# Kernel optimization log

Hardware: AMD Instinct MI355X
Metric: run time of the kernel (lower is better)

Reference implementation:

```python
import jax, jax.numpy as jnp
import numpy as np

N_NODES = 100000
N_EDGES = 3200000
N_FEAT = 128
EMB = 64
HID = 64
N_SUB = 500000
N_GRAPHS = 1024
BN_EPS = 1e-5


def setup_inputs() -> dict:
    key = jax.random.key(0)
    ks = jax.random.split(key, 12)
    full_x = jax.random.normal(ks[0], (N_NODES, N_FEAT), dtype=jnp.float32)
    full_edge_index = jax.random.randint(ks[1], (2, N_EDGES), 0, N_NODES, dtype=jnp.int64)
    subgraph_node_indices = jax.random.randint(ks[2], (N_SUB,), 0, N_NODES, dtype=jnp.int64)
    batch_vector = jax.random.randint(ks[3], (N_SUB,), 0, N_GRAPHS, dtype=jnp.int64)
    # GCNConv params (glorot-style scale)
    W_enc = jax.random.normal(ks[4], (N_FEAT, EMB), dtype=jnp.float32) * (1.0 / np.sqrt(N_FEAT))
    b_enc = jnp.zeros((EMB,), dtype=jnp.float32)
    # predictor MLP params
    W1 = jax.random.normal(ks[5], (EMB, HID), dtype=jnp.float32) * (1.0 / np.sqrt(EMB))
    b1 = jnp.zeros((HID,), dtype=jnp.float32)
    gamma = jnp.ones((HID,), dtype=jnp.float32)
    beta = jnp.zeros((HID,), dtype=jnp.float32)
    W2 = jax.random.normal(ks[6], (HID, 1), dtype=jnp.float32) * (1.0 / np.sqrt(HID))
    b2 = jnp.zeros((1,), dtype=jnp.float32)
    return {
        "full_x": full_x,
        "full_edge_index": full_edge_index,
        "subgraph_node_indices": subgraph_node_indices,
        "batch_vector": batch_vector,
        "W_enc": W_enc, "b_enc": b_enc,
        "W1": W1, "b1": b1, "gamma": gamma, "beta": beta,
        "W2": W2, "b2": b2,
    }


def gcn_conv(x, edge_index, W, b):
    # PyG GCNConv: add self-loops, symmetric degree normalization, linear transform
    n = x.shape[0]
    loops = jnp.arange(n, dtype=edge_index.dtype)
    row = jnp.concatenate([edge_index[0], loops])  # source
    col = jnp.concatenate([edge_index[1], loops])  # target
    deg = jax.ops.segment_sum(jnp.ones_like(col, dtype=x.dtype), col, num_segments=n)
    dinv = jnp.where(deg > 0, jax.lax.rsqrt(deg), 0.0)
    norm = dinv[row] * dinv[col]  # [E+N]
    xw = x @ W  # transform first: [N, EMB]
    msgs = xw[row] * norm[:, None]
    out = jax.ops.segment_sum(msgs, col, num_segments=n)
    return out + b


def reference(full_x, full_edge_index, subgraph_node_indices, batch_vector,
              W_enc, b_enc, W1, b1, gamma, beta, W2, b2):
    # encoder + relu over all nodes
    h = jax.nn.relu(gcn_conv(full_x, full_edge_index, W_enc, b_enc))  # [N, EMB]
    # gather subgraph members
    sub = h[subgraph_node_indices]  # [N_SUB, EMB]
    # segment-mean pool into per-subgraph embeddings
    sums = jax.ops.segment_sum(sub, batch_vector, num_segments=N_GRAPHS)
    cnts = jax.ops.segment_sum(jnp.ones((sub.shape[0],), sub.dtype), batch_vector, num_segments=N_GRAPHS)
    pooled = sums / jnp.maximum(cnts, 1.0)[:, None]  # [N_GRAPHS, EMB]
    # predictor: Linear -> ReLU -> BatchNorm1d (training-mode batch stats) -> Linear
    z = jax.nn.relu(pooled @ W1 + b1)  # [N_GRAPHS, HID]
    mu = jnp.mean(z, axis=0)
    var = jnp.mean((z - mu) ** 2, axis=0)  # biased, as torch BN normalization
    zn = (z - mu) * jax.lax.rsqrt(var + BN_EPS) * gamma + beta
    return zn @ W2 + b2  # [N_GRAPHS, 1]
```

## Files before the change

### kernel.cpp

```cpp
#include <hip/hip_runtime.h>

#define N_NODES 100000
#define N_EDGES 3200000
#define N_FEAT 128
#define EMB 64
#define HID 64
#define N_SUB 500000
#define N_GRAPHS 1024
#define BN_EPS 1e-5f

#define NBKT 782
#define TILE 4096
#define NTILES 782
#define NGTILES 123
#define BKT_MAX 4864
#define GCAP 640

typedef __attribute__((ext_vector_type(8))) short short8;
typedef __attribute__((ext_vector_type(8))) unsigned short ushort8v;
typedef __attribute__((ext_vector_type(4))) float floatx4;

#define OFF_BCUR   0u
#define OFF_BCURG  4096u
#define OFF_BNSUM  8192u
#define ZERO_BYTES 8704u
#define OFF_DINV   12288u
#define OFF_OFFS   412672u
#define OFF_PAIRS  812672u
#define OFF_XWS    OFF_PAIRS
#define OFF_CSR    16027264u
#define OFF_SORTED 31241856u
#define OFF_H      33863296u
#define OFF_Z      46663296u

__device__ __forceinline__ bool is_bf(const unsigned* gamma_raw) {
  return (gamma_raw[0] & 0xFFFFu) != 0u;
}
__device__ __forceinline__ bool idx_is64(const int* subp) {
  return (subp[1] | subp[3] | subp[5] | subp[7]) == 0;
}
__device__ __forceinline__ int ld_idx(const int* p, long long i, bool w64) {
  return w64 ? p[2 * i] : p[i];
}
__device__ __forceinline__ float bf2f(ushort u) {
  union { unsigned i; float f; } v; v.i = ((unsigned)u) << 16; return v.f;
}
__device__ __forceinline__ ushort f2bf(float f) {
  union { float f; unsigned i; } v; v.f = f;
  unsigned lsb = (v.i >> 16) & 1u;
  v.i += 0x7FFFu + lsb;
  return (ushort)(v.i >> 16);
}
__device__ __forceinline__ float ld_f(const void* p, int i, bool bf) {
  return bf ? bf2f(((const ushort*)p)[i]) : ((const float*)p)[i];
}

__global__ void k_scatsort(const int* e, const int* subp, const int* batch,
                           int* bcur, unsigned* pairs, int* bcurg, int* sorted) {
  __shared__ char smem[38912];
  int* cnt   = (int*)smem;
  int* lscan = cnt + 1024;
  int* gbase = lscan + 1024;
  int* psum  = gbase + 1024;
  unsigned* stage = (unsigned*)(psum + 512);
  unsigned short* stgb = (unsigned short*)(stage + 4096);
  bool w64 = idx_is64(subp);
  int tid = threadIdx.x;
  bool edges = blockIdx.x < NTILES;
  int nb   = edges ? NBKT : N_GRAPHS;
  int base = edges ? blockIdx.x * TILE : (blockIdx.x - NTILES) * TILE;
  int tot  = edges ? N_EDGES : N_SUB;
  int tcnt = min(TILE, tot - base);
  for (int i = tid; i < nb; i += 512) cnt[i] = 0;
  __syncthreads();
  if (edges) {
    for (int j = tid; j < tcnt; j += 512) {
      int tgt = ld_idx(e, (long long)N_EDGES + base + j, w64);
      atomicAdd(&cnt[tgt >> 7], 1);
    }
  } else {
    for (int j = tid; j < tcnt; j += 512)
      atomicAdd(&cnt[ld_idx(batch, base + j, w64)], 1);
  }
  __syncthreads();
  int b0 = tid * 2, v0 = 0, v1 = 0, s = 0;
  if (b0 < nb) {
    v0 = cnt[b0];
    v1 = (b0 + 1 < nb) ? cnt[b0 + 1] : 0;
    s = v0 + v1;
  }
  psum[tid] = s;
  __syncthreads();
  for (int d = 1; d < 512; d <<= 1) {
    int t = (tid >= d) ? psum[tid - d] : 0; __syncthreads();
    psum[tid] += t; __syncthreads();
  }
  if (b0 < nb) {
    int excl = psum[tid] - s;
    lscan[b0] = excl;
    if (b0 + 1 < nb) lscan[b0 + 1] = excl + v0;
  }
  __syncthreads();
  if (edges) {
    for (int b = tid; b < nb; b += 512) {
      int c = cnt[b];
      gbase[b] = c ? b * BKT_MAX + atomicAdd(&bcur[b], c) : 0;
      cnt[b] = 0;
    }
  } else {
    for (int b = tid; b < nb; b += 512) {
      int c = cnt[b];
      gbase[b] = c ? b * GCAP + atomicAdd(&bcurg[b], c) : 0;
      cnt[b] = 0;
    }
  }
  __syncthreads();
  if (edges) {
    for (int j = tid; j < tcnt; j += 512) {
      int ei = base + j;
      int src = ld_idx(e, ei, w64);
      int tgt = ld_idx(e, (long long)N_EDGES + ei, w64);
      int b = tgt >> 7;
      int r = atomicAdd(&cnt[b], 1);
      int p = lscan[b] + r;
      stage[p] = ((unsigned)(tgt & 127) << 20) | (unsigned)src;
      stgb[p] = (unsigned short)b;
    }
  } else {
    for (int j = tid; j < tcnt; j += 512) {
      int g = ld_idx(batch, base + j, w64);
      int nid = ld_idx(subp, base + j, w64);
      int r = atomicAdd(&cnt[g], 1);
      int p = lscan[g] + r;
      stage[p] = (unsigned)nid;
      stgb[p] = (unsigned short)g;
    }
  }
  __syncthreads();
  if (edges) {
    for (int j = tid; j < tcnt; j += 512) {
      int b = stgb[j];
      pairs[gbase[b] + (j - lscan[b])] = stage[j];
    }
  } else {
    for (int j = tid; j < tcnt; j += 512) {
      int b = stgb[j];
      sorted[gbase[b] + (j - lscan[b])] = (int)stage[j];
    }
  }
}

__global__ void k_csr(const unsigned* __restrict__ pairs, const int* __restrict__ bcur,
                      int* __restrict__ csr, unsigned* __restrict__ offs,
                      float* __restrict__ dinv) {
  __shared__ int dl[128], loff[128], lcur[128];
  __shared__ int stage[BKT_MAX];
  int tid = threadIdx.x, b = blockIdx.x;
  if (tid < 128) dl[tid] = 0;
  __syncthreads();
  int s = b * BKT_MAX, cnt = bcur[b];
  {
    int j = tid;
    unsigned pn = (j < cnt) ? pairs[s + j] : 0u;
    for (; j < cnt; j += 512) {
      unsigned p = pn;
      int jn = j + 512;
      pn = (jn < cnt) ? pairs[s + jn] : 0u;
      atomicAdd(&dl[p >> 20], 1);
    }
  }
  __syncthreads();
  if (tid < 128) loff[tid] = dl[tid];
  __syncthreads();
  for (int d = 1; d < 128; d <<= 1) {
    int t = (tid >= d && tid < 128) ? loff[tid - d] : 0;
    __syncthreads();
    if (tid < 128) loff[tid] += t;
    __syncthreads();
  }
  if (tid < 128) {
    int deg = dl[tid];
    int excl = loff[tid] - deg;
    lcur[tid] = excl;
    int n = b * 128 + tid;
    if (n < N_NODES) {
      offs[n] = ((unsigned)deg << 24) | (unsigned)(s + excl);
      dinv[n] = rsqrtf((float)(deg + 1));
    }
  }
  __syncthreads();
  {
    int j = tid;
    unsigned pn = (j < cnt) ? pairs[s + j] : 0u;
    for (; j < cnt; j += 512) {
      unsigned p = pn;
      int jn = j + 512;
      pn = (jn < cnt) ? pairs[s + jn] : 0u;
      int pos = atomicAdd(&lcur[p >> 20], 1);
      stage[pos] = (int)(p & 0xFFFFF);
    }
  }
  __syncthreads();
  for (int j = tid; j < cnt; j += 512) csr[s + j] = stage[j];
}

__global__ void k_gemm(const void* xraw, const void* Wraw, const unsigned* gamu,
                       const float* __restrict__ dinv, ushort* __restrict__ xws) {
  bool bf = is_bf(gamu);
  const ushort* Wus = (const ushort*)Wraw;
  const float*  Wf  = (const float*)Wraw;
  int wv = threadIdx.x >> 6, lane = threadIdx.x & 63;
  int m = lane & 15, quad = lane >> 4;
  int c0 = wv * 16;
  short8 bfrag[4];
#pragma unroll
  for (int kc = 0; kc < 4; ++kc)
#pragma unroll
    for (int j = 0; j < 8; ++j) {
      int idx = (kc * 32 + quad * 8 + j) * EMB + c0 + m;
      bfrag[kc][j] = (short)(bf ? Wus[idx] : f2bf(Wf[idx]));
    }
  const ushort* xs = (const ushort*)xraw;
  const float*  xf = (const float*)xraw;
  for (int t = blockIdx.x; t < N_NODES / 16; t += gridDim.x) {
    int r0 = t * 16;
    floatx4 acc = {0.f, 0.f, 0.f, 0.f};
    if (bf) {
#pragma unroll
      for (int kc = 0; kc < 4; ++kc) {
        short8 a = *(const short8*)(xs + (r0 + m) * N_FEAT + kc * 32 + quad * 8);
        acc = __builtin_amdgcn_mfma_f32_16x16x32_bf16(a, bfrag[kc], acc, 0, 0, 0);
      }
    } else {
#pragma unroll
      for (int kc = 0; kc < 4; ++kc) {
        const float* ap = xf + (r0 + m) * N_FEAT + kc * 32 + quad * 8;
        float4 f0 = *(const float4*)ap, f1 = *(const float4*)(ap + 4);
        short8 a;
        a[0] = (short)f2bf(f0.x); a[1] = (short)f2bf(f0.y);
        a[2] = (short)f2bf(f0.z); a[3] = (short)f2bf(f0.w);
        a[4] = (short)f2bf(f1.x); a[5] = (short)f2bf(f1.y);
        a[6] = (short)f2bf(f1.z); a[7] = (short)f2bf(f1.w);
        acc = __builtin_amdgcn_mfma_f32_16x16x32_bf16(a, bfrag[kc], acc, 0, 0, 0);
      }
    }
#pragma unroll
    for (int r = 0; r < 4; ++r) {
      int row = r0 + quad * 4 + r;
      xws[row * EMB + c0 + m] = f2bf(acc[r] * dinv[row]);
    }
  }
}

#define ACC8(u) { a0 += bf2f(u[0]); a1 += bf2f(u[1]); a2 += bf2f(u[2]); a3 += bf2f(u[3]); \
                  a4 += bf2f(u[4]); a5 += bf2f(u[5]); a6 += bf2f(u[6]); a7 += bf2f(u[7]); }

__global__ void k_agg(const ushort* __restrict__ xws, const float* __restrict__ dinv,
                      const unsigned* __restrict__ offs, const int* __restrict__ csr,
                      const void* benc, const unsigned* gamu, ushort* __restrict__ h) {
  bool bf = is_bf(gamu);
  int wv = threadIdx.x >> 6, lane = threadIdx.x & 63;
  int e8 = lane >> 3, q = lane & 7;
  int n = blockIdx.x * 4 + wv;
  unsigned w = offs[n];
  int start = (int)(w & 0xFFFFFFu), end = start + (int)(w >> 24);
  float a0 = 0.f, a1 = 0.f, a2 = 0.f, a3 = 0.f, a4 = 0.f, a5 = 0.f, a6 = 0.f, a7 = 0.f;
  int i = start;
  for (; i + 31 < end; i += 32) {
    const int* cp = csr + i;
    int s0 = cp[e8], s1 = cp[8 + e8], s2 = cp[16 + e8], s3 = cp[24 + e8];
    ushort8v u0 = *(const ushort8v*)(xws + s0 * 64 + q * 8);
    ushort8v u1 = *(const ushort8v*)(xws + s1 * 64 + q * 8);
    ushort8v u2 = *(const ushort8v*)(xws + s2 * 64 + q * 8);
    ushort8v u3 = *(const ushort8v*)(xws + s3 * 64 + q * 8);
    ACC8(u0) ACC8(u1) ACC8(u2) ACC8(u3)
  }
  for (; i < end; i += 8) {
    if (i + e8 < end) {
      int s0 = csr[i + e8];
      ushort8v u0 = *(const ushort8v*)(xws + s0 * 64 + q * 8);
      ACC8(u0)
    }
  }
#pragma unroll
  for (int msk = 8; msk < 64; msk <<= 1) {
    a0 += __shfl_xor(a0, msk); a1 += __shfl_xor(a1, msk);
    a2 += __shfl_xor(a2, msk); a3 += __shfl_xor(a3, msk);
    a4 += __shfl_xor(a4, msk); a5 += __shfl_xor(a5, msk);
    a6 += __shfl_xor(a6, msk); a7 += __shfl_xor(a7, msk);
  }
  float dn = dinv[n];
  ushort8v us = *(const ushort8v*)(xws + n * 64 + q * 8);
  if (e8 == 0) {
    ushort8v o;
    o[0] = f2bf(fmaxf((a0 + bf2f(us[0])) * dn + ld_f(benc, q * 8 + 0, bf), 0.f));
    o[1] = f2bf(fmaxf((a1 + bf2f(us[1])) * dn + ld_f(benc, q * 8 + 1, bf), 0.f));
    o[2] = f2bf(fmaxf((a2 + bf2f(us[2])) * dn + ld_f(benc, q * 8 + 2, bf), 0.f));
    o[3] = f2bf(fmaxf((a3 + bf2f(us[3])) * dn + ld_f(benc, q * 8 + 3, bf), 0.f));
    o[4] = f2bf(fmaxf((a4 + bf2f(us[4])) * dn + ld_f(benc, q * 8 + 4, bf), 0.f));
    o[5] = f2bf(fmaxf((a5 + bf2f(us[5])) * dn + ld_f(benc, q * 8 + 5, bf), 0.f));
    o[6] = f2bf(fmaxf((a6 + bf2f(us[6])) * dn + ld_f(benc, q * 8 + 6, bf), 0.f));
    o[7] = f2bf(fmaxf((a7 + bf2f(us[7])) * dn + ld_f(benc, q * 8 + 7, bf), 0.f));
    *(ushort8v*)(h + n * 64 + q * 8) = o;
  }
}

__global__ void k_poolmlp1(const ushort* __restrict__ h, const int* __restrict__ sorted,
                           const int* __restrict__ bcurg, const void* W1, const void* b1,
                           const unsigned* gamu, float* __restrict__ z, float* bn) {
  bool bf = is_bf(gamu);
  __shared__ float red[4 * 64];
  __shared__ float pl[64];
  int g = blockIdx.x;
  int tid = threadIdx.x, wv = tid >> 6, lane = tid & 63;
  int e8 = lane >> 3, q = lane & 7;
  int start = g * GCAP, cnt = bcurg[g];
  int end = start + cnt;
  float a0 = 0.f, a1 = 0.f, a2 = 0.f, a3 = 0.f, a4 = 0.f, a5 = 0.f, a6 = 0.f, a7 = 0.f;
  for (int i = start + wv * 16; i < end; i += 64) {
    if (i + e8 < end) {
      int n0 = sorted[i + e8];
      ushort8v u = *(const ushort8v*)(h + n0 * 64 + q * 8);
      ACC8(u)
    }
    if (i + 8 + e8 < end) {
      int n1 = sorted[i + 8 + e8];
      ushort8v u = *(const ushort8v*)(h + n1 * 64 + q * 8);
      ACC8(u)
    }
  }
#pragma unroll
  for (int msk = 8; msk < 64; msk <<= 1) {
    a0 += __shfl_xor(a0, msk); a1 += __shfl_xor(a1, msk);
    a2 += __shfl_xor(a2, msk); a3 += __shfl_xor(a3, msk);
    a4 += __shfl_xor(a4, msk); a5 += __shfl_xor(a5, msk);
    a6 += __shfl_xor(a6, msk); a7 += __shfl_xor(a7, msk);
  }
  if (e8 == 0) {
    float* r = red + wv * 64 + q * 8;
    r[0] = a0; r[1] = a1; r[2] = a2; r[3] = a3;
    r[4] = a4; r[5] = a5; r[6] = a6; r[7] = a7;
  }
  __syncthreads();
  if (tid < 64) {
    float s = red[tid] + red[64 + tid] + red[128 + tid] + red[192 + tid];
    pl[tid] = s / fmaxf((float)cnt, 1.f);
  }
  __syncthreads();
  if (tid < 64) {
    int f = tid;
    float acc = ld_f(b1, f, bf);
#pragma unroll 8
    for (int k = 0; k < HID; ++k) acc += pl[k] * ld_f(W1, k * HID + f, bf);
    float zv = fmaxf(acc, 0.f);
    z[g * HID + f] = zv;
    atomicAdd(&bn[f], zv);
    atomicAdd(&bn[HID + f], zv * zv);
  }
}

__global__ void k_mlp2(const float* __restrict__ z, const float* __restrict__ bn,
                       const void* gmm, const void* beta, const void* W2, const void* b2,
                       const unsigned* gamu, void* out) {
  bool bf = is_bf(gamu);
  int wv = threadIdx.x >> 6, f = threadIdx.x & 63;
  int g = blockIdx.x * 4 + wv;
  float mu = bn[f] * (1.f / N_GRAPHS);
  float var = bn[HID + f] * (1.f / N_GRAPHS) - mu * mu;
  float zn = (z[g * HID + f] - mu) * rsqrtf(var + BN_EPS) * ld_f(gmm, f, bf) + ld_f(beta, f, bf);
  float val = zn * ld_f(W2, f, bf);
  for (int off = 32; off; off >>= 1) val += __shfl_down(val, off);
  if (f == 0) {
    val += ld_f(b2, 0, bf);
    if (bf) ((ushort*)out)[g] = f2bf(val);
    else    ((float*)out)[g]  = val;
  }
}

extern "C" void kernel_launch(void* const* d_in, const int* in_sizes, int n_in,
                              void* d_out, int out_size, void* d_ws, size_t ws_size,
                              hipStream_t stream) {
  const void* x_raw    = d_in[0];
  const int*  e_raw    = (const int*)d_in[1];
  const int*  sub_raw  = (const int*)d_in[2];
  const int*  bat_raw  = (const int*)d_in[3];
  const void* Wenc     = d_in[4];
  const void* benc     = d_in[5];
  const void* W1       = d_in[6];
  const void* b1       = d_in[7];
  const unsigned* gamu = (const unsigned*)d_in[8];
  const void* beta     = d_in[9];
  const void* W2       = d_in[10];
  const void* b2       = d_in[11];

  char* ws = (char*)d_ws;
  int*      bcur   = (int*)(ws + OFF_BCUR);
  int*      bcurg  = (int*)(ws + OFF_BCURG);
  float*    bnsum  = (float*)(ws + OFF_BNSUM);
  float*    dinv   = (float*)(ws + OFF_DINV);
  unsigned* offs   = (unsigned*)(ws + OFF_OFFS);
  unsigned* pairs  = (unsigned*)(ws + OFF_PAIRS);
  ushort*   xws    = (ushort*)(ws + OFF_XWS);
  int*      csr    = (int*)(ws + OFF_CSR);
  int*      sorted = (int*)(ws + OFF_SORTED);
  ushort*   h      = (ushort*)(ws + OFF_H);
  float*    z      = (float*)(ws + OFF_Z);

  hipMemsetAsync(ws, 0, ZERO_BYTES, stream);

  k_scatsort<<<NTILES + NGTILES, 512, 0, stream>>>(e_raw, sub_raw, bat_raw,
                                                   bcur, pairs, bcurg, sorted);
  k_csr     <<<NBKT, 512, 0, stream>>>(pairs, bcur, csr, offs, dinv);
  k_gemm    <<<1024, 256, 0, stream>>>(x_raw, Wenc, gamu, dinv, xws);
  k_agg     <<<N_NODES / 4, 256, 0, stream>>>(xws, dinv, offs, csr, benc, gamu, h);
  k_poolmlp1<<<N_GRAPHS, 256, 0, stream>>>(h, sorted, bcurg, W1, b1, gamu, z, bnsum);
  k_mlp2    <<<N_GRAPHS / 4, 256, 0, stream>>>(z, bnsum, gamu, beta, W2, b2, gamu, d_out);
}
```

Before: 298.3 us.

## Use wave-shuffle scan, branchless padded gathers, and wider pooling loads

```diff
diff --git a/kernel.cpp b/kernel.cpp
--- a/kernel.cpp
+++ b/kernel.cpp
@@ -15,6 +15,7 @@
 #define NGTILES 123
 #define BKT_MAX 4864
 #define GCAP 640
+#define ZROW 100000
 
 typedef __attribute__((ext_vector_type(8))) short short8;
 typedef __attribute__((ext_vector_type(8))) unsigned short ushort8v;
@@ -57,15 +58,15 @@
 
 __global__ void k_scatsort(const int* e, const int* subp, const int* batch,
                            int* bcur, unsigned* pairs, int* bcurg, int* sorted) {
-  __shared__ char smem[38912];
+  __shared__ char smem[36896];
   int* cnt   = (int*)smem;
   int* lscan = cnt + 1024;
   int* gbase = lscan + 1024;
-  int* psum  = gbase + 1024;
-  unsigned* stage = (unsigned*)(psum + 512);
+  int* wsum  = gbase + 1024;
+  unsigned* stage = (unsigned*)(wsum + 8);
   unsigned short* stgb = (unsigned short*)(stage + 4096);
   bool w64 = idx_is64(subp);
-  int tid = threadIdx.x;
+  int tid = threadIdx.x, lane = tid & 63, wv = tid >> 6;
   bool edges = blockIdx.x < NTILES;
   int nb   = edges ? NBKT : N_GRAPHS;
   int base = edges ? blockIdx.x * TILE : (blockIdx.x - NTILES) * TILE;
@@ -74,13 +75,20 @@
   for (int i = tid; i < nb; i += 512) cnt[i] = 0;
   __syncthreads();
   if (edges) {
-    for (int j = tid; j < tcnt; j += 512) {
-      int tgt = ld_idx(e, (long long)N_EDGES + base + j, w64);
-      atomicAdd(&cnt[tgt >> 7], 1);
+    if (w64) {
+      const int2* tp = (const int2*)e + (size_t)N_EDGES + base;
+      for (int j = tid; j < tcnt; j += 512) atomicAdd(&cnt[tp[j].x >> 7], 1);
+    } else {
+      for (int j = tid; j < tcnt; j += 512)
+        atomicAdd(&cnt[e[N_EDGES + base + j] >> 7], 1);
     }
   } else {
-    for (int j = tid; j < tcnt; j += 512)
-      atomicAdd(&cnt[ld_idx(batch, base + j, w64)], 1);
+    if (w64) {
+      const int2* bp = (const int2*)batch + base;
+      for (int j = tid; j < tcnt; j += 512) atomicAdd(&cnt[bp[j].x], 1);
+    } else {
+      for (int j = tid; j < tcnt; j += 512) atomicAdd(&cnt[batch[base + j]], 1);
+    }
   }
   __syncthreads();
   int b0 = tid * 2, v0 = 0, v1 = 0, s = 0;
@@ -89,37 +97,40 @@
     v1 = (b0 + 1 < nb) ? cnt[b0 + 1] : 0;
     s = v0 + v1;
   }
-  psum[tid] = s;
-  __syncthreads();
-  for (int d = 1; d < 512; d <<= 1) {
-    int t = (tid >= d) ? psum[tid - d] : 0; __syncthreads();
-    psum[tid] += t; __syncthreads();
-  }
+  int val = s;
+#pragma unroll
+  for (int d = 1; d < 64; d <<= 1) {
+    int t = __shfl_up(val, d);
+    if (lane >= d) val += t;
+  }
+  if (lane == 63) wsum[wv] = val;
+  __syncthreads();
+  int woff = 0;
+#pragma unroll
+  for (int w = 0; w < 8; ++w) woff += (w < wv) ? wsum[w] : 0;
   if (b0 < nb) {
-    int excl = psum[tid] - s;
+    int excl = (val + woff) - s;
     lscan[b0] = excl;
     if (b0 + 1 < nb) lscan[b0 + 1] = excl + v0;
   }
   __syncthreads();
-  if (edges) {
-    for (int b = tid; b < nb; b += 512) {
-      int c = cnt[b];
-      gbase[b] = c ? b * BKT_MAX + atomicAdd(&bcur[b], c) : 0;
-      cnt[b] = 0;
-    }
-  } else {
-    for (int b = tid; b < nb; b += 512) {
-      int c = cnt[b];
-      gbase[b] = c ? b * GCAP + atomicAdd(&bcurg[b], c) : 0;
-      cnt[b] = 0;
-    }
+  for (int b = tid; b < nb; b += 512) {
+    int c = cnt[b];
+    gbase[b] = c ? (edges ? b * BKT_MAX + atomicAdd(&bcur[b], c)
+                          : b * GCAP + atomicAdd(&bcurg[b], c)) : 0;
+    cnt[b] = 0;
   }
   __syncthreads();
   if (edges) {
     for (int j = tid; j < tcnt; j += 512) {
-      int ei = base + j;
-      int src = ld_idx(e, ei, w64);
-      int tgt = ld_idx(e, (long long)N_EDGES + ei, w64);
+      int src, tgt;
+      if (w64) {
+        src = ((const int2*)e)[base + j].x;
+        tgt = ((const int2*)e)[(size_t)N_EDGES + base + j].x;
+      } else {
+        src = e[base + j];
+        tgt = e[N_EDGES + base + j];
+      }
       int b = tgt >> 7;
       int r = atomicAdd(&cnt[b], 1);
       int p = lscan[b] + r;
@@ -128,8 +139,14 @@
     }
   } else {
     for (int j = tid; j < tcnt; j += 512) {
-      int g = ld_idx(batch, base + j, w64);
-      int nid = ld_idx(subp, base + j, w64);
+      int g, nid;
+      if (w64) {
+        g = ((const int2*)batch)[base + j].x;
+        nid = ((const int2*)subp)[base + j].x;
+      } else {
+        g = batch[base + j];
+        nid = subp[base + j];
+      }
       int r = atomicAdd(&cnt[g], 1);
       int p = lscan[g] + r;
       stage[p] = (unsigned)nid;
@@ -206,6 +223,8 @@
 
 __global__ void k_gemm(const void* xraw, const void* Wraw, const unsigned* gamu,
                        const float* __restrict__ dinv, ushort* __restrict__ xws) {
+  if (blockIdx.x == 0 && threadIdx.x < 32)
+    ((unsigned*)xws)[(unsigned)ZROW * 32u + threadIdx.x] = 0u;
   bool bf = is_bf(gamu);
   const ushort* Wus = (const ushort*)Wraw;
   const float*  Wf  = (const float*)Wraw;
@@ -254,6 +273,10 @@
 
 #define ACC8(u) { a0 += bf2f(u[0]); a1 += bf2f(u[1]); a2 += bf2f(u[2]); a3 += bf2f(u[3]); \
                   a4 += bf2f(u[4]); a5 += bf2f(u[5]); a6 += bf2f(u[6]); a7 += bf2f(u[7]); }
+#define FMA8(u, sc) { a0 = fmaf(sc, bf2f(u[0]), a0); a1 = fmaf(sc, bf2f(u[1]), a1); \
+                      a2 = fmaf(sc, bf2f(u[2]), a2); a3 = fmaf(sc, bf2f(u[3]), a3); \
+                      a4 = fmaf(sc, bf2f(u[4]), a4); a5 = fmaf(sc, bf2f(u[5]), a5); \
+                      a6 = fmaf(sc, bf2f(u[6]), a6); a7 = fmaf(sc, bf2f(u[7]), a7); }
 
 __global__ void k_agg(const ushort* __restrict__ xws, const float* __restrict__ dinv,
                       const unsigned* __restrict__ offs, const int* __restrict__ csr,
@@ -265,22 +288,18 @@
   unsigned w = offs[n];
   int start = (int)(w & 0xFFFFFFu), end = start + (int)(w >> 24);
   float a0 = 0.f, a1 = 0.f, a2 = 0.f, a3 = 0.f, a4 = 0.f, a5 = 0.f, a6 = 0.f, a7 = 0.f;
-  int i = start;
-  for (; i + 31 < end; i += 32) {
-    const int* cp = csr + i;
-    int s0 = cp[e8], s1 = cp[8 + e8], s2 = cp[16 + e8], s3 = cp[24 + e8];
+  for (int i = start; i < end; i += 32) {
+    int i0 = i + e8, i1 = i0 + 8, i2 = i0 + 16, i3 = i0 + 24;
+    int l0 = csr[i0], l1 = csr[i1], l2 = csr[i2], l3 = csr[i3];
+    int s0 = (i0 < end) ? l0 : ZROW;
+    int s1 = (i1 < end) ? l1 : ZROW;
+    int s2 = (i2 < end) ? l2 : ZROW;
+    int s3 = (i3 < end) ? l3 : ZROW;
     ushort8v u0 = *(const ushort8v*)(xws + s0 * 64 + q * 8);
     ushort8v u1 = *(const ushort8v*)(xws + s1 * 64 + q * 8);
     ushort8v u2 = *(const ushort8v*)(xws + s2 * 64 + q * 8);
     ushort8v u3 = *(const ushort8v*)(xws + s3 * 64 + q * 8);
     ACC8(u0) ACC8(u1) ACC8(u2) ACC8(u3)
-  }
-  for (; i < end; i += 8) {
-    if (i + e8 < end) {
-      int s0 = csr[i + e8];
-      ushort8v u0 = *(const ushort8v*)(xws + s0 * 64 + q * 8);
-      ACC8(u0)
-    }
   }
 #pragma unroll
   for (int msk = 8; msk < 64; msk <<= 1) {
@@ -317,16 +336,15 @@
   int start = g * GCAP, cnt = bcurg[g];
   int end = start + cnt;
   float a0 = 0.f, a1 = 0.f, a2 = 0.f, a3 = 0.f, a4 = 0.f, a5 = 0.f, a6 = 0.f, a7 = 0.f;
-  for (int i = start + wv * 16; i < end; i += 64) {
-    if (i + e8 < end) {
-      int n0 = sorted[i + e8];
-      ushort8v u = *(const ushort8v*)(h + n0 * 64 + q * 8);
-      ACC8(u)
-    }
-    if (i + 8 + e8 < end) {
-      int n1 = sorted[i + 8 + e8];
-      ushort8v u = *(const ushort8v*)(h + n1 * 64 + q * 8);
-      ACC8(u)
+  for (int i = start + wv * 32; i < end; i += 128) {
+#pragma unroll
+    for (int c = 0; c < 4; ++c) {
+      int idx = i + c * 8 + e8;
+      int safe = min(idx, end - 1);
+      int nn = sorted[safe];
+      float sc = (idx < end) ? 1.f : 0.f;
+      ushort8v u = *(const ushort8v*)(h + nn * 64 + q * 8);
+      FMA8(u, sc)
     }
   }
 #pragma unroll
```

Result: no change. 292.7 us (-1.9%).
